# Kernel tuning notes

Measured on AMD Instinct MI355X. Metric: run time of the kernel, lower is better.

Reference implementation:

```python
import jax, jax.numpy as jnp
import numpy as np

SEQ, D, HID, C = 512, 768, 128, 5
NENT, SPAN = 128, 16


def setup_inputs() -> dict:
    key = jax.random.key(0)
    ks = jax.random.split(key, 24)
    s = 0.02

    def rn(k, shape, scale=s):
        return jax.random.normal(k, shape, dtype=jnp.float32) * scale

    inp = {
        "encoder_output": rn(ks[0], (1, SEQ, D), 1.0),
        "holder_idxs": jax.random.randint(ks[1], (NENT, SPAN), 0, SEQ, dtype=jnp.int32),
        "target_idxs": jax.random.randint(ks[2], (NENT, SPAN), 0, SEQ, dtype=jnp.int32),
        "exp_idxs": jax.random.randint(ks[3], (NENT, SPAN), 0, SEQ, dtype=jnp.int32),
    }
    names = ["Wh_f", "bh_f", "Wh_b", "bh_b", "Wt_f", "bt_f", "Wt_b", "bt_b",
             "We_f", "be_f", "We_b", "be_b"]
    for n, k in zip(names, ks[4:16]):
        shape = (4 * HID, D) if n.startswith("W") else (4 * HID,)
        inp[n] = rn(k, shape)
    inp["T_he"] = rn(ks[16], (2 * HID, 2 * HID, 2 * HID))
    inp["T_te"] = rn(ks[17], (2 * HID, 2 * HID, 2 * HID))
    inp["T_cls"] = rn(ks[18], (2 * HID, C, 2 * HID))
    return inp


def _lstm_cell_step(x, W_ih, b):
    # Single LSTM step with h0=c0=0 (the torch module feeds seq_len=1 to nn.LSTM,
    # so W_hh @ h0 vanishes; b = b_ih + b_hh). Gate order: i, f, g, o.
    g = x @ W_ih.T + b                         # [n, L, 4H]
    i, f, gg, o = jnp.split(g, 4, axis=-1)
    c = jax.nn.sigmoid(i) * jnp.tanh(gg)
    return jax.nn.sigmoid(o) * jnp.tanh(c)     # h, [n, L, H]


def _lstm_pool(enc_seq, idxs, Wf, bf, Wb, bb):
    toks = enc_seq[idxs]                       # [n, L, D] gather
    h = jnp.concatenate([_lstm_cell_step(toks, Wf, bf),
                         _lstm_cell_step(toks, Wb, bb)], axis=-1)  # [n, L, 2H]
    return h.max(axis=1)                       # max-pool over span -> [n, 2H]


def reference(encoder_output, holder_idxs, target_idxs, exp_idxs,
              Wh_f, bh_f, Wh_b, bh_b, Wt_f, bt_f, Wt_b, bt_b,
              We_f, be_f, We_b, be_b, T_he, T_te, T_cls):
    enc = encoder_output[0]                    # [SEQ, D]
    He = _lstm_pool(enc, holder_idxs, Wh_f, bh_f, Wh_b, bh_b)   # [nh, 2H]
    Te = _lstm_pool(enc, target_idxs, Wt_f, bt_f, Wt_b, bt_b)   # [nt, 2H]
    Ee = _lstm_pool(enc, exp_idxs, We_f, be_f, We_b, be_b)      # [ne, 2H]

    # hep[i,k] = He[i] @ T_he @ Ee[k];  tep[j,k] = Te[j] @ T_te @ Ee[k]
    hep = jnp.einsum('ia,abc,kc->ikb', He, T_he, Ee)            # [nh, ne, 2H]
    tep = jnp.einsum('ja,abc,kc->jkb', Te, T_te, Ee)            # [nt, ne, 2H]
    # pred[i,j,k,m] = tep[j,k] @ T_cls[:,m,:] @ hep[i,k]
    pred = jnp.einsum('jkb,bmc,ikc->ijkm', tep, T_cls, hep)     # [nh, nt, ne, C]
    return pred
```

## Files before the change

### kernel.cpp

```cpp
#include <hip/hip_runtime.h>
#include <hip/hip_bf16.h>
#include <math.h>

#define DIM   768
#define HID   128
#define H2    256
#define NENT  128
#define SPAN  16
#define NCLS  5

#define POOLB_OFF  0
#define TCLSB_OFF  196608
#define HEPT_OFF   851968
#define TEPT_OFF   9240576
#define HEPN_OFF   17629184
#define TEPN_OFF   26017792
#define GATESB_OFF 17629184
#define PREDT_OFF  17629184
#define WB_OFF     59572224
#define TOKB_OFF   63111168

typedef __attribute__((ext_vector_type(8))) short bf16x8;
typedef __attribute__((ext_vector_type(4))) float f32x4;

__device__ __forceinline__ float sigmoidf_(float x) { return 1.0f / (1.0f + __expf(-x)); }

__device__ __forceinline__ unsigned short f2bf(float x) {
    __hip_bfloat16 h = __float2bfloat16(x);
    return *reinterpret_cast<unsigned short*>(&h);
}
__device__ __forceinline__ float bf2f(unsigned short u) {
    unsigned int v = ((unsigned int)u) << 16;
    float f; __builtin_memcpy(&f, &v, 4); return f;
}

__global__ __launch_bounds__(256)
void prep_kernel(const float* __restrict__ Whf, const float* __restrict__ Whb,
                 const float* __restrict__ Wtf, const float* __restrict__ Wtb,
                 const float* __restrict__ Wef, const float* __restrict__ Web,
                 const float* __restrict__ Tcls, const float* __restrict__ enc,
                 const int* __restrict__ idx_h, const int* __restrict__ idx_t,
                 const int* __restrict__ idx_e,
                 unsigned short* __restrict__ WB, unsigned short* __restrict__ TB,
                 unsigned short* __restrict__ tokB)
{
    const int bb = blockIdx.x;
    const int tid = threadIdx.x;
    if (bb < 1728) {
        int gid = bb * 256 + tid;
        int t2  = gid / 73728;
        int rem = gid % 73728;
        int n   = rem / 192;
        int c4  = rem % 192;
        int gate = n >> 7, j = n & 127;
        int srow = (gate == 0) ? j : (gate == 1) ? 256 + j : 384 + j;
        const float* W = (t2 == 0) ? Whf : (t2 == 1) ? Whb : (t2 == 2) ? Wtf :
                         (t2 == 3) ? Wtb : (t2 == 4) ? Wef : Web;
        float4 v = ((const float4*)(W + srow * DIM))[c4];
        unsigned short* d = WB + ((size_t)(t2 * 384 + n)) * DIM + c4 * 4;
        d[0] = f2bf(v.x); d[1] = f2bf(v.y); d[2] = f2bf(v.z); d[3] = f2bf(v.w);
    } else if (bb < 3008) {
        int idx = (bb - 1728) * 256 + tid;
        int b = idx / (NCLS * H2);
        int r = idx % (NCLS * H2);
        int m = r >> 8, c = r & 255;
        TB[((m << 8) + c) * H2 + b] = f2bf(Tcls[idx]);
    } else {
        int gid = (bb - 3008) * 256 + tid;
        int r  = gid / 192, c4 = gid % 192;
        int type = r >> 11;
        int rem  = r & 2047;
        const int* idx = (type == 0) ? idx_h : (type == 1) ? idx_t : idx_e;
        int row = idx[rem];
        float4 v = ((const float4*)(enc + (size_t)row * DIM))[c4];
        unsigned short h4[4] = { f2bf(v.x), f2bf(v.y), f2bf(v.z), f2bf(v.w) };
        *(uint2*)(tokB + (size_t)r * DIM + c4 * 4) = *(uint2*)h4;
    }
}

__global__ __launch_bounds__(256)
void gates_mfma(const unsigned short* __restrict__ tokB,
                const unsigned short* __restrict__ WB,
                unsigned short* __restrict__ gatesB)
{
    __shared__ unsigned short As[2][128 * 64];
    __shared__ unsigned short Bs[2][128 * 64];
    const int lbid = ((int)blockIdx.x & 7) * 36 + ((int)blockIdx.x >> 3);
    const int type = lbid / 96;
    const int rem  = lbid % 96;
    const int mb0  = (rem / 6) * 128;
    const int nb0  = (rem % 6) * 128;
    const int tid = threadIdx.x;
    const int w = tid >> 6, l = tid & 63;
    const int lr = l & 15, lg = l >> 4;
    const unsigned short* A = tokB + (size_t)type * 2048 * DIM + (size_t)mb0 * DIM;
    const unsigned short* B = WB   + (size_t)type * 768  * DIM + (size_t)nb0 * DIM;

    const int sr0 = tid >> 3;
    const int sc  = tid & 7;

    bf16x8 ra[4], rb[4];
    #define LOADT(kt)                                                        \
        {                                                                    \
            const int koff = (kt) * 64 + sc * 8;                             \
            _Pragma("unroll")                                                \
            for (int p = 0; p < 4; ++p) {                                    \
                int rr = sr0 + p * 32;                                       \
                ra[p] = *(const bf16x8*)(A + (size_t)rr * DIM + koff);       \
                rb[p] = *(const bf16x8*)(B + (size_t)rr * DIM + koff);       \
            }                                                                \
        }
    #define WRITET(buf)                                                      \
        {                                                                    \
            _Pragma("unroll")                                                \
            for (int p = 0; p < 4; ++p) {                                    \
                int rr = sr0 + p * 32;                                       \
                int bo = (rr * 128 + sc * 16) ^ ((rr & 7) << 4);             \
                *(bf16x8*)((char*)As[buf] + bo) = ra[p];                     \
                *(bf16x8*)((char*)Bs[buf] + bo) = rb[p];                     \
            }                                                                \
        }

    f32x4 acc[4][4];
    #pragma unroll
    for (int mt = 0; mt < 4; ++mt)
        #pragma unroll
        for (int nt = 0; nt < 4; ++nt) acc[mt][nt] = (f32x4){0.f, 0.f, 0.f, 0.f};

    const int am0 = (w & 1) * 64;
    const int bn0 = (w >> 1) * 64;

    LOADT(0);
    WRITET(0);
    __syncthreads();

    int cur = 0;
    #pragma unroll 1
    for (int kt = 0; kt < 12; ++kt) {
        if (kt + 1 < 12) LOADT(kt + 1);

        #pragma unroll
        for (int ks = 0; ks < 2; ++ks) {
            bf16x8 af[4], bf[4];
            #pragma unroll
            for (int mt = 0; mt < 4; ++mt) {
                int rr = am0 + mt * 16 + lr;
                int bo = (rr * 128 + ks * 64 + lg * 16) ^ ((rr & 7) << 4);
                af[mt] = *(const bf16x8*)((const char*)As[cur] + bo);
            }
            #pragma unroll
            for (int nt = 0; nt < 4; ++nt) {
                int rr = bn0 + nt * 16 + lr;
                int bo = (rr * 128 + ks * 64 + lg * 16) ^ ((rr & 7) << 4);
                bf[nt] = *(const bf16x8*)((const char*)Bs[cur] + bo);
            }
            #pragma unroll
            for (int mt = 0; mt < 4; ++mt)
                #pragma unroll
                for (int nt = 0; nt < 4; ++nt)
                    acc[mt][nt] = __builtin_amdgcn_mfma_f32_16x16x32_bf16(af[mt], bf[nt], acc[mt][nt], 0, 0, 0);
        }

        if (kt + 1 < 12) {
            WRITET(cur ^ 1);
        }
        __syncthreads();
        cur ^= 1;
    }
    #undef LOADT
    #undef WRITET

    unsigned short* C = gatesB + (size_t)type * 2048 * 768 + (size_t)mb0 * 768 + nb0;
    #pragma unroll
    for (int mt = 0; mt < 4; ++mt)
        #pragma unroll
        for (int nt = 0; nt < 4; ++nt)
            #pragma unroll
            for (int r = 0; r < 4; ++r)
                C[(size_t)(am0 + mt * 16 + lg * 4 + r) * 768 + bn0 + nt * 16 + lr] = f2bf(acc[mt][nt][r]);
}

__global__ __launch_bounds__(256)
void pool_epilogue(const unsigned short* __restrict__ gatesB,
                   const float* __restrict__ bhf, const float* __restrict__ bhb,
                   const float* __restrict__ btf, const float* __restrict__ btb,
                   const float* __restrict__ bef, const float* __restrict__ beb,
                   unsigned short* __restrict__ poolB)
{
    const int type = blockIdx.x >> 7;
    const int ent  = blockIdx.x & 127;
    const int tid  = threadIdx.x;
    const int dir  = tid >> 7;
    const int j    = tid & 127;
    const float* Bv = (type == 0) ? (dir ? bhb : bhf)
                    : (type == 1) ? (dir ? btb : btf)
                                  : (dir ? beb : bef);
    const float bi = Bv[j], bg = Bv[2 * HID + j], bo = Bv[3 * HID + j];
    const unsigned short* g0 = gatesB + ((size_t)type * 2048 + ent * 16) * 768 + dir * 384 + j;
    float hmax = -1e30f;
    #pragma unroll
    for (int ll = 0; ll < SPAN; ++ll) {
        const unsigned short* gr = g0 + ll * 768;
        float iv = sigmoidf_(bf2f(gr[0])   + bi);
        float gv = tanhf(   bf2f(gr[128]) + bg);
        float ov = sigmoidf_(bf2f(gr[256]) + bo);
        hmax = fmaxf(hmax, ov * tanhf(iv * gv));
    }
    poolB[(size_t)(type * NENT + ent) * H2 + dir * HID + j] = f2bf(hmax);
}

__global__ __launch_bounds__(1024)
void pair_mfma(const unsigned short* __restrict__ EeB,
               const unsigned short* __restrict__ HeB,
               const unsigned short* __restrict__ TeB,
               const float* __restrict__ T0, const float* __restrict__ T1,
               unsigned short* __restrict__ hepN,
               unsigned short* __restrict__ tepN)
{
    __shared__ __align__(16) char smem[131072];
    const int bid = blockIdx.x;
    const int t = bid >> 8;
    const int b = bid & 255;
    const float* T = t ? T1 : T0;
    const unsigned short* Hx = t ? TeB : HeB;
    unsigned short* outp = t ? tepN : hepN;
    const int tid = threadIdx.x;
    const int w = tid >> 6, l = tid & 63;
    const int lr = l & 15, lg = l >> 4;

    {
        const int r0 = tid >> 5;
        const int ch = tid & 31;
        #pragma unroll
        for (int p = 0; p < 8; ++p) {
            int row = p * 32 + r0;
            const float* src = T + ((size_t)row * 256 + b) * 256 + ch * 8;
            float4 v0 = ((const float4*)src)[0];
            float4 v1 = ((const float4*)src)[1];
            bf16x8 hv; unsigned short* hp = (unsigned short*)&hv;
            hp[0]=f2bf(v0.x); hp[1]=f2bf(v0.y); hp[2]=f2bf(v0.z); hp[3]=f2bf(v0.w);
            hp[4]=f2bf(v1.x); hp[5]=f2bf(v1.y); hp[6]=f2bf(v1.z); hp[7]=f2bf(v1.w);
            int bo = (row * 512 + ch * 16) ^ ((row & 7) << 4);
            *(bf16x8*)(smem + bo) = hv;
        }
    }
    __syncthreads();

    f32x4 acc1[4][2];
    {
        const int aw = (w & 3) * 64;
        const int kw = (w >> 2) * 32;
        #pragma unroll
        for (int mt = 0; mt < 4; ++mt)
            #pragma unroll
            for (int nt = 0; nt < 2; ++nt) acc1[mt][nt] = (f32x4){0.f, 0.f, 0.f, 0.f};

        #pragma unroll
        for (int ks = 0; ks < 8; ++ks) {
            bf16x8 af[4], bf[2];
            #pragma unroll
            for (int mt = 0; mt < 4; ++mt) {
                int ar = aw + mt * 16 + lr;
                int bo = (ar * 512 + (ks * 32 + lg * 8) * 2) ^ ((ar & 7) << 4);
                af[mt] = *(const bf16x8*)(smem + bo);
            }
            #pragma unroll
            for (int nt = 0; nt < 2; ++nt)
                bf[nt] = *(const bf16x8*)(EeB + (kw + nt * 16 + lr) * H2 + ks * 32 + lg * 8);
            #pragma unroll
            for (int mt = 0; mt < 4; ++mt)
                #pragma unroll
                for (int nt = 0; nt < 2; ++nt)
                    acc1[mt][nt] = __builtin_amdgcn_mfma_f32_16x16x32_bf16(af[mt], bf[nt], acc1[mt][nt], 0, 0, 0);
        }
    }
    __syncthreads();

    {
        const int aw = (w & 3) * 64;
        const int kw = (w >> 2) * 32;
        #pragma unroll
        for (int mt = 0; mt < 4; ++mt)
            #pragma unroll
            for (int nt = 0; nt < 2; ++nt) {
                int k  = kw + nt * 16 + lr;
                int a0 = aw + mt * 16 + lg * 4;
                unsigned short h4[4] = { f2bf(acc1[mt][nt][0]), f2bf(acc1[mt][nt][1]),
                                         f2bf(acc1[mt][nt][2]), f2bf(acc1[mt][nt][3]) };
                int bo = (k * 512 + a0 * 2) ^ ((k & 7) << 4);
                *(uint2*)(smem + bo) = *(uint2*)h4;
            }
    }
    __syncthreads();

    {
        const int kw2 = (w >> 3) * 64;
        const int iw  = (w & 7) * 16;
        f32x4 acc2[4];
        #pragma unroll
        for (int mt = 0; mt < 4; ++mt) acc2[mt] = (f32x4){0.f, 0.f, 0.f, 0.f};

        #pragma unroll
        for (int ks = 0; ks < 8; ++ks) {
            bf16x8 af[4], bf;
            #pragma unroll
            for (int mt = 0; mt < 4; ++mt) {
                int kr = kw2 + mt * 16 + lr;
                int bo = (kr * 512 + (ks * 32 + lg * 8) * 2) ^ ((kr & 7) << 4);
                af[mt] = *(const bf16x8*)(smem + bo);
            }
            bf = *(const bf16x8*)(Hx + (iw + lr) * H2 + ks * 32 + lg * 8);
            #pragma unroll
            for (int mt = 0; mt < 4; ++mt)
                acc2[mt] = __builtin_amdgcn_mfma_f32_16x16x32_bf16(af[mt], bf, acc2[mt], 0, 0, 0);
        }
        unsigned short* po = outp + (size_t)b * (128 * 128);
        #pragma unroll
        for (int mt = 0; mt < 4; ++mt)
            #pragma unroll
            for (int r = 0; r < 4; ++r) {
                int k = kw2 + mt * 16 + lg * 4 + r;
                int i = iw + lr;
                po[k * 128 + i] = f2bf(acc2[mt][r]);
            }
    }
}

__global__ __launch_bounds__(256)
void trT(const unsigned short* __restrict__ hepN, const unsigned short* __restrict__ tepN,
         unsigned short* __restrict__ hepT, unsigned short* __restrict__ tepT)
{
    __shared__ unsigned short L[128 * 256];
    const int t = blockIdx.x >> 7;
    const int k = blockIdx.x & 127;
    const unsigned short* src = t ? tepN : hepN;
    unsigned short* dst = (t ? tepT : hepT) + (size_t)k * 32768;
    const int tid = threadIdx.x;

    #pragma unroll
    for (int it = 0; it < 16; ++it) {
        int g = it * 256 + tid;
        int b = g >> 4, i8 = g & 15;
        bf16x8 v = *(const bf16x8*)(src + (size_t)b * 16384 + k * 128 + i8 * 8);
        #pragma unroll
        for (int e = 0; e < 8; ++e) {
            int i = i8 * 8 + e;
            int bo = (i * 512 + b * 2) ^ ((i8 & 7) << 4);
            *(unsigned short*)((char*)L + bo) = ((unsigned short*)&v)[e];
        }
    }
    __syncthreads();

    #pragma unroll
    for (int it = 0; it < 16; ++it) {
        int h = it * 256 + tid;
        int i = h >> 5, ch = h & 31;
        int bo = (i * 512 + ch * 16) ^ (((i >> 3) & 7) << 4);
        bf16x8 v = *(const bf16x8*)((const char*)L + bo);
        *(bf16x8*)(dst + i * 256 + ch * 8) = v;
    }
}

__global__ __launch_bounds__(512)
void step3v2(const unsigned short* __restrict__ hepT,
             const unsigned short* __restrict__ tepT,
             const unsigned short* __restrict__ TclsB,
             float* __restrict__ predT)
{
    __shared__ unsigned short tepS[32 * 256];
    __shared__ unsigned short WS[32 * 256];
    const int lbid = ((int)blockIdx.x & 7) * 64 + ((int)blockIdx.x >> 3);
    const int k  = lbid >> 2;
    const int jq = lbid & 3;
    const int j0 = jq * 32;
    const int tid = threadIdx.x;
    const int w = tid >> 6, l = tid & 63;
    const int lr = l & 15, lg = l >> 4;

    #pragma unroll
    for (int it = 0; it < 2; ++it) {
        int g = it * 512 + tid;
        int row = g >> 5, ch = g & 31;
        bf16x8 v = *(const bf16x8*)(tepT + ((size_t)k * 128 + j0 + row) * 256 + ch * 8);
        int bo = (row * 512 + ch * 16) ^ ((row & 7) << 4);
        *(bf16x8*)((char*)tepS + bo) = v;
    }

    bf16x8 ha[8];
    #pragma unroll
    for (int ks = 0; ks < 8; ++ks)
        ha[ks] = *(const bf16x8*)(hepT + ((size_t)k * 128 + w * 16 + lr) * 256 + ks * 32 + lg * 8);
    __syncthreads();

    #pragma unroll 1
    for (int m = 0; m < NCLS; ++m) {
        {
            const unsigned short* tcm = TclsB + (size_t)m * (H2 * H2);
            f32x4 a1[2][2];
            #pragma unroll
            for (int jt = 0; jt < 2; ++jt)
                #pragma unroll
                for (int ct = 0; ct < 2; ++ct) a1[jt][ct] = (f32x4){0.f, 0.f, 0.f, 0.f};

            #pragma unroll
            for (int ks = 0; ks < 8; ++ks) {
                bf16x8 a[2], bb[2];
                #pragma unroll
                for (int jt = 0; jt < 2; ++jt) {
                    int bo = ((jt * 16 + lr) * 512 + (ks * 32 + lg * 8) * 2) ^ ((lr & 7) << 4);
                    a[jt] = *(const bf16x8*)((const char*)tepS + bo);
                }
                #pragma unroll
                for (int ct = 0; ct < 2; ++ct)
                    bb[ct] = *(const bf16x8*)(tcm + (size_t)(w * 32 + ct * 16 + lr) * H2 + ks * 32 + lg * 8);
                #pragma unroll
                for (int jt = 0; jt < 2; ++jt)
                    #pragma unroll
                    for (int ct = 0; ct < 2; ++ct)
                        a1[jt][ct] = __builtin_amdgcn_mfma_f32_16x16x32_bf16(a[jt], bb[ct], a1[jt][ct], 0, 0, 0);
            }
            #pragma unroll
            for (int jt = 0; jt < 2; ++jt)
                #pragma unroll
                for (int ct = 0; ct < 2; ++ct)
                    #pragma unroll
                    for (int r = 0; r < 4; ++r) {
                        int j = jt * 16 + lg * 4 + r;
                        int c = w * 32 + ct * 16 + lr;
                        int bo = (j * 512 + c * 2) ^ ((j & 7) << 4);
                        *(unsigned short*)((char*)WS + bo) = f2bf(a1[jt][ct][r]);
                    }
        }
        __syncthreads();

        {
            f32x4 a2[2];
            #pragma unroll
            for (int jt = 0; jt < 2; ++jt) a2[jt] = (f32x4){0.f, 0.f, 0.f, 0.f};

            #pragma unroll
            for (int ks = 0; ks < 8; ++ks) {
                #pragma unroll
                for (int jt = 0; jt < 2; ++jt) {
                    int bo = ((jt * 16 + lr) * 512 + (ks * 32 + lg * 8) * 2) ^ ((lr & 7) << 4);
                    bf16x8 wb = *(const bf16x8*)((const char*)WS + bo);
                    a2[jt] = __builtin_amdgcn_mfma_f32_16x16x32_bf16(ha[ks], wb, a2[jt], 0, 0, 0);
                }
            }
            float* po = predT + (size_t)(k * NCLS + m) * (NENT * NENT);
            #pragma unroll
            for (int jt = 0; jt < 2; ++jt)
                #pragma unroll
                for (int r = 0; r < 4; ++r) {
                    int i = w * 16 + lg * 4 + r;
                    int j = j0 + jt * 16 + lr;
                    po[i * NENT + j] = a2[jt][r];
                }
        }
        __syncthreads();
    }
}

__global__ __launch_bounds__(256)
void transpose_out(const float* __restrict__ predT, float* __restrict__ out)
{
    __shared__ float Ls[160][33];
    const int bid = blockIdx.x;
    const int ij0 = (bid >> 2) * 32;
    const int km0 = (bid & 3) * 160;
    const int t = threadIdx.x;

    #pragma unroll
    for (int q = 0; q < 20; ++q) {
        int r = (t >> 5) + q * 8;
        int c = t & 31;
        Ls[r][c] = predT[(size_t)(km0 + r) * 16384 + ij0 + c];
    }
    __syncthreads();
    for (int idx = t; idx < 32 * 160; idx += 256) {
        int r = idx / 160, c = idx % 160;
        out[(size_t)(ij0 + r) * 640 + km0 + c] = Ls[c][r];
    }
}

extern "C" void kernel_launch(void* const* d_in, const int* in_sizes, int n_in,
                              void* d_out, int out_size, void* d_ws, size_t ws_size,
                              hipStream_t stream)
{
    (void)in_sizes; (void)n_in; (void)out_size; (void)ws_size;
    const float* enc  = (const float*)d_in[0];
    const int*   hidx = (const int*)d_in[1];
    const int*   tidx = (const int*)d_in[2];
    const int*   eidx = (const int*)d_in[3];
    const float* Whf = (const float*)d_in[4];
    const float* bhf = (const float*)d_in[5];
    const float* Whb = (const float*)d_in[6];
    const float* bhb = (const float*)d_in[7];
    const float* Wtf = (const float*)d_in[8];
    const float* btf = (const float*)d_in[9];
    const float* Wtb = (const float*)d_in[10];
    const float* btb = (const float*)d_in[11];
    const float* Wef = (const float*)d_in[12];
    const float* bef = (const float*)d_in[13];
    const float* Web = (const float*)d_in[14];
    const float* beb = (const float*)d_in[15];
    const float* T_he  = (const float*)d_in[16];
    const float* T_te  = (const float*)d_in[17];
    const float* T_cls = (const float*)d_in[18];

    float* out = (float*)d_out;
    char*  ws  = (char*)d_ws;
    unsigned short* poolB  = (unsigned short*)(ws + POOLB_OFF);
    unsigned short* TclsB  = (unsigned short*)(ws + TCLSB_OFF);
    unsigned short* hepT   = (unsigned short*)(ws + HEPT_OFF);
    unsigned short* tepT   = (unsigned short*)(ws + TEPT_OFF);
    unsigned short* hepN   = (unsigned short*)(ws + HEPN_OFF);
    unsigned short* tepN   = (unsigned short*)(ws + TEPN_OFF);
    unsigned short* gatesB = (unsigned short*)(ws + GATESB_OFF);
    float*          predT  = (float*)(ws + PREDT_OFF);
    unsigned short* WB     = (unsigned short*)(ws + WB_OFF);
    unsigned short* tokB   = (unsigned short*)(ws + TOKB_OFF);

    unsigned short* HeB = poolB;
    unsigned short* TeB = poolB + 1 * NENT * H2;
    unsigned short* EeB = poolB + 2 * NENT * H2;

    prep_kernel<<<7616, 256, 0, stream>>>(Whf, Whb, Wtf, Wtb, Wef, Web,
                                          T_cls, enc, hidx, tidx, eidx,
                                          WB, TclsB, tokB);

    gates_mfma<<<288, 256, 0, stream>>>(tokB, WB, gatesB);

    pool_epilogue<<<384, 256, 0, stream>>>(gatesB, bhf, bhb, btf, btb, bef, beb, poolB);

    pair_mfma<<<512, 1024, 0, stream>>>(EeB, HeB, TeB, T_he, T_te, hepN, tepN);

    trT<<<256, 256, 0, stream>>>(hepN, tepN, hepT, tepT);

    step3v2<<<512, 512, 0, stream>>>(hepT, tepT, TclsB, predT);

    transpose_out<<<2048, 256, 0, stream>>>(predT, out);
}
```

Baseline: 152.6 us.

## Fuse hep/tep transpose into step3 loads and drop separate transpose kernel

Removes the standalone trT kernel that transposed hepN/tepN into hepT/tepT through global memory. Instead, step3v3 reads the untransposed layouts directly and transposes them through swizzled shared memory while staging. The hep operand is transposed in two 64-row halves through a shared buffer that is later reused as WS, so each half needs extra barriers. This saves a kernel launch and a full write-then-read of the transposed intermediates. In exchange the global reads are strided and short (64–256 B per row), and each of the four j-quarter blocks per k re-reads the whole hep slice.

```diff
diff --git a/kernel.cpp b/kernel.cpp
--- a/kernel.cpp
+++ b/kernel.cpp
@@ -11,10 +11,8 @@
 
 #define POOLB_OFF  0
 #define TCLSB_OFF  196608
-#define HEPT_OFF   851968
-#define TEPT_OFF   9240576
-#define HEPN_OFF   17629184
-#define TEPN_OFF   26017792
+#define HEPN_OFF   851968
+#define TEPN_OFF   9240576
 #define GATESB_OFF 17629184
 #define PREDT_OFF  17629184
 #define WB_OFF     59572224
@@ -326,49 +324,16 @@
     }
 }
 
-__global__ __launch_bounds__(256)
-void trT(const unsigned short* __restrict__ hepN, const unsigned short* __restrict__ tepN,
-         unsigned short* __restrict__ hepT, unsigned short* __restrict__ tepT)
-{
-    __shared__ unsigned short L[128 * 256];
-    const int t = blockIdx.x >> 7;
-    const int k = blockIdx.x & 127;
-    const unsigned short* src = t ? tepN : hepN;
-    unsigned short* dst = (t ? tepT : hepT) + (size_t)k * 32768;
-    const int tid = threadIdx.x;
-
-    #pragma unroll
-    for (int it = 0; it < 16; ++it) {
-        int g = it * 256 + tid;
-        int b = g >> 4, i8 = g & 15;
-        bf16x8 v = *(const bf16x8*)(src + (size_t)b * 16384 + k * 128 + i8 * 8);
-        #pragma unroll
-        for (int e = 0; e < 8; ++e) {
-            int i = i8 * 8 + e;
-            int bo = (i * 512 + b * 2) ^ ((i8 & 7) << 4);
-            *(unsigned short*)((char*)L + bo) = ((unsigned short*)&v)[e];
-        }
-    }
-    __syncthreads();
-
-    #pragma unroll
-    for (int it = 0; it < 16; ++it) {
-        int h = it * 256 + tid;
-        int i = h >> 5, ch = h & 31;
-        int bo = (i * 512 + ch * 16) ^ (((i >> 3) & 7) << 4);
-        bf16x8 v = *(const bf16x8*)((const char*)L + bo);
-        *(bf16x8*)(dst + i * 256 + ch * 8) = v;
-    }
-}
-
 __global__ __launch_bounds__(512)
-void step3v2(const unsigned short* __restrict__ hepT,
-             const unsigned short* __restrict__ tepT,
+void step3v3(const unsigned short* __restrict__ hepN,
+             const unsigned short* __restrict__ tepN,
              const unsigned short* __restrict__ TclsB,
              float* __restrict__ predT)
 {
-    __shared__ unsigned short tepS[32 * 256];
-    __shared__ unsigned short WS[32 * 256];
+    __shared__ __align__(16) char smem[49152];
+    char* tepS = smem;
+    char* bufA = smem + 16384;
+    char* WS   = smem + 16384;
     const int lbid = ((int)blockIdx.x & 7) * 64 + ((int)blockIdx.x >> 3);
     const int k  = lbid >> 2;
     const int jq = lbid & 3;
@@ -380,16 +345,60 @@
     #pragma unroll
     for (int it = 0; it < 2; ++it) {
         int g = it * 512 + tid;
-        int row = g >> 5, ch = g & 31;
-        bf16x8 v = *(const bf16x8*)(tepT + ((size_t)k * 128 + j0 + row) * 256 + ch * 8);
-        int bo = (row * 512 + ch * 16) ^ ((row & 7) << 4);
-        *(bf16x8*)((char*)tepS + bo) = v;
+        int b = g & 255, j8 = g >> 8;
+        bf16x8 v = *(const bf16x8*)(tepN + (size_t)b * 16384 + k * 128 + j0 + j8 * 8);
+        #pragma unroll
+        for (int e = 0; e < 8; ++e) {
+            int j = j8 * 8 + e;
+            int bo = (j * 512 + b * 2) ^ (e << 4);
+            *(unsigned short*)(tepS + bo) = ((unsigned short*)&v)[e];
+        }
     }
 
     bf16x8 ha[8];
     #pragma unroll
-    for (int ks = 0; ks < 8; ++ks)
-        ha[ks] = *(const bf16x8*)(hepT + ((size_t)k * 128 + w * 16 + lr) * 256 + ks * 32 + lg * 8);
+    for (int it = 0; it < 4; ++it) {
+        int g = it * 512 + tid;
+        int b = g & 255, i8 = g >> 8;
+        bf16x8 v = *(const bf16x8*)(hepN + (size_t)b * 16384 + k * 128 + i8 * 8);
+        #pragma unroll
+        for (int e = 0; e < 8; ++e) {
+            int il = i8 * 8 + e;
+            int bo = (il * 512 + b * 2) ^ (e << 4);
+            *(unsigned short*)(bufA + bo) = ((unsigned short*)&v)[e];
+        }
+    }
+    __syncthreads();
+    if (w < 4) {
+        int il = (w & 3) * 16 + lr;
+        #pragma unroll
+        for (int ks = 0; ks < 8; ++ks) {
+            int bo = (il * 512 + (ks * 32 + lg * 8) * 2) ^ ((il & 7) << 4);
+            ha[ks] = *(const bf16x8*)(bufA + bo);
+        }
+    }
+    __syncthreads();
+    #pragma unroll
+    for (int it = 0; it < 4; ++it) {
+        int g = it * 512 + tid;
+        int b = g & 255, i8 = g >> 8;
+        bf16x8 v = *(const bf16x8*)(hepN + (size_t)b * 16384 + k * 128 + 64 + i8 * 8);
+        #pragma unroll
+        for (int e = 0; e < 8; ++e) {
+            int il = i8 * 8 + e;
+            int bo = (il * 512 + b * 2) ^ (e << 4);
+            *(unsigned short*)(bufA + bo) = ((unsigned short*)&v)[e];
+        }
+    }
+    __syncthreads();
+    if (w >= 4) {
+        int il = (w & 3) * 16 + lr;
+        #pragma unroll
+        for (int ks = 0; ks < 8; ++ks) {
+            int bo = (il * 512 + (ks * 32 + lg * 8) * 2) ^ ((il & 7) << 4);
+            ha[ks] = *(const bf16x8*)(bufA + bo);
+        }
+    }
     __syncthreads();
 
     #pragma unroll 1
@@ -408,7 +417,7 @@
                 #pragma unroll
                 for (int jt = 0; jt < 2; ++jt) {
                     int bo = ((jt * 16 + lr) * 512 + (ks * 32 + lg * 8) * 2) ^ ((lr & 7) << 4);
-                    a[jt] = *(const bf16x8*)((const char*)tepS + bo);
+                    a[jt] = *(const bf16x8*)(tepS + bo);
                 }
                 #pragma unroll
                 for (int ct = 0; ct < 2; ++ct)
@@ -428,7 +437,7 @@
                         int j = jt * 16 + lg * 4 + r;
                         int c = w * 32 + ct * 16 + lr;
                         int bo = (j * 512 + c * 2) ^ ((j & 7) << 4);
-                        *(unsigned short*)((char*)WS + bo) = f2bf(a1[jt][ct][r]);
+                        *(unsigned short*)(WS + bo) = f2bf(a1[jt][ct][r]);
                     }
         }
         __syncthreads();
@@ -443,7 +452,7 @@
                 #pragma unroll
                 for (int jt = 0; jt < 2; ++jt) {
                     int bo = ((jt * 16 + lr) * 512 + (ks * 32 + lg * 8) * 2) ^ ((lr & 7) << 4);
-                    bf16x8 wb = *(const bf16x8*)((const char*)WS + bo);
+                    bf16x8 wb = *(const bf16x8*)(WS + bo);
                     a2[jt] = __builtin_amdgcn_mfma_f32_16x16x32_bf16(ha[ks], wb, a2[jt], 0, 0, 0);
                 }
             }
@@ -512,8 +521,6 @@
     char*  ws  = (char*)d_ws;
     unsigned short* poolB  = (unsigned short*)(ws + POOLB_OFF);
     unsigned short* TclsB  = (unsigned short*)(ws + TCLSB_OFF);
-    unsigned short* hepT   = (unsigned short*)(ws + HEPT_OFF);
-    unsigned short* tepT   = (unsigned short*)(ws + TEPT_OFF);
     unsigned short* hepN   = (unsigned short*)(ws + HEPN_OFF);
     unsigned short* tepN   = (unsigned short*)(ws + TEPN_OFF);
     unsigned short* gatesB = (unsigned short*)(ws + GATESB_OFF);
@@ -535,9 +542,7 @@
 
     pair_mfma<<<512, 1024, 0, stream>>>(EeB, HeB, TeB, T_he, T_te, hepN, tepN);
 
-    trT<<<256, 256, 0, stream>>>(hepN, tepN, hepT, tepT);
-
-    step3v2<<<512, 512, 0, stream>>>(hepT, tepT, TclsB, predT);
+    step3v3<<<512, 512, 0, stream>>>(hepN, tepN, TclsB, predT);
 
     transpose_out<<<2048, 256, 0, stream>>>(predT, out);
 }
```

Measured after the change: 147.7 us. 3.2% less time.
